# Kernel tuning notes

Measured on AMD Instinct MI355X. Metric: run time of the kernel, lower is better.

The kernel has to match this reference:

```python
import jax, jax.numpy as jnp
import numpy as np

N = 8192
D = 512


def setup_inputs() -> dict:
    key = jax.random.key(0)
    k1, k2, k3, k4 = jax.random.split(key, 4)
    U = jax.random.normal(k1, (N, D), dtype=jnp.float32)
    V = jax.random.normal(k2, (N, D), dtype=jnp.float32)
    M = jax.random.normal(k3, (N, N), dtype=jnp.float32)
    W = jax.random.uniform(k4, (N, N), dtype=jnp.float32)
    alpha = jnp.ones((1,), dtype=jnp.float32) * 0.1
    return {"U": U, "V": V, "M": M, "W": W, "alpha": alpha}


def reference(U, V, M, W, alpha):
    # Reconstruction term: sum((U V^T - M)^2)
    recon = U @ V.T                                  # (N, N) GEMM
    part1 = jnp.sum(jnp.square(recon - M))
    # Manifold term in closed form:
    # sum_{i,j} W[i,j] * ||U_i - V_j||^2
    #   = sum_i rowW_i ||U_i||^2 + sum_j colW_j ||V_j||^2 - 2 sum(W * U V^T)
    u_sq = jnp.sum(U * U, axis=1)                    # (N,)
    v_sq = jnp.sum(V * V, axis=1)                    # (N,)
    row_w = jnp.sum(W, axis=1)                       # (N,)
    col_w = jnp.sum(W, axis=0)                       # (N,)
    cross = jnp.sum(W * recon)
    part2 = alpha[0] * (jnp.dot(row_w, u_sq) + jnp.dot(col_w, v_sq) - 2.0 * cross)
    total = part1 + part2
    return total / (M.shape[0] * M.shape[1])
```

## Files before the change

### kernel.cpp

```cpp
#include <hip/hip_runtime.h>
#include <hip/hip_bf16.h>
#include <stdint.h>

#define N_DIM 8192
#define D_DIM 512
#define BM 128
#define BN 128
#define BK 64
#define RSTR 140

typedef __attribute__((ext_vector_type(8))) short bf16x8;
typedef __attribute__((ext_vector_type(4))) float f32x4;

__device__ __forceinline__ unsigned short f2bf(float f) {
    unsigned int x = __float_as_uint(f);
    x += 0x7fffu + ((x >> 16) & 1u);
    return (unsigned short)(x >> 16);
}
__device__ __forceinline__ float bf2f(unsigned short u) {
    return __uint_as_float(((unsigned int)u) << 16);
}

__global__ void __launch_bounds__(256) prep_kernel(
    const float* __restrict__ U, const float* __restrict__ V,
    unsigned short* __restrict__ Ub, unsigned short* __restrict__ Vb,
    float* __restrict__ usq, float* __restrict__ vsq)
{
    int row = blockIdx.x;
    const float* src;
    unsigned short* dst;
    float* sq;
    if (row < N_DIM) {
        src = U + (size_t)row * D_DIM;
        dst = Ub + (size_t)row * D_DIM;
        sq  = usq + row;
    } else {
        int r = row - N_DIM;
        src = V + (size_t)r * D_DIM;
        dst = Vb + (size_t)r * D_DIM;
        sq  = vsq + r;
    }
    int t = threadIdx.x;
    float2 v = *reinterpret_cast<const float2*>(src + 2 * t);
    float s = v.x * v.x + v.y * v.y;
    ushort2 b;
    b.x = f2bf(v.x);
    b.y = f2bf(v.y);
    *reinterpret_cast<ushort2*>(dst + 2 * t) = b;

    #pragma unroll
    for (int o = 32; o > 0; o >>= 1) s += __shfl_down(s, o, 64);
    __shared__ float red[4];
    if ((t & 63) == 0) red[t >> 6] = s;
    __syncthreads();
    if (t == 0) *sq = red[0] + red[1] + red[2] + red[3];
}

__global__ void __launch_bounds__(256, 2) fused_kernel(
    const unsigned short* __restrict__ Ub, const unsigned short* __restrict__ Vb,
    const float* __restrict__ Mg, const float* __restrict__ Wg,
    const float* __restrict__ usq, const float* __restrict__ vsq,
    double* __restrict__ acc)
{
    __shared__ alignas(16) char smem[BM * BK * 2 + BN * BK * 2];
    __shared__ alignas(16) unsigned short recs[BM * RSTR];
    __shared__ float red1[4], red2[4];
    char* As = smem;
    char* Bs = smem + BM * BK * 2;

    const int t    = threadIdx.x;
    const int lane = t & 63;
    const int wave = t >> 6;
    const int wm   = wave >> 1;
    const int wn   = wave & 1;

    const int bid    = blockIdx.x;
    const int tile_m = bid >> 6;
    const int tile_n = bid & 63;
    const int row0   = tile_m * BM;
    const int col0   = tile_n * BN;

    const f32x4 zero = {0.f, 0.f, 0.f, 0.f};
    f32x4 a[4][4];
    #pragma unroll
    for (int i = 0; i < 4; ++i)
        #pragma unroll
        for (int j = 0; j < 4; ++j) a[i][j] = zero;

    auto As3 = (__attribute__((address_space(3))) char*)As;
    auto Bs3 = (__attribute__((address_space(3))) char*)Bs;

    for (int kt = 0; kt < D_DIM / BK; ++kt) {
        const int k0 = kt * BK;
        #pragma unroll
        for (int c = 0; c < 4; ++c) {
            int s   = c * 256 + t;
            int row = s >> 3;
            int kg  = s & 7;
            int kgs = kg ^ (row & 7);
            __builtin_amdgcn_global_load_lds(
                (const __attribute__((address_space(1))) void*)(Ub + (size_t)(row0 + row) * D_DIM + k0 + kgs * 8),
                (__attribute__((address_space(3))) void*)(As3 + s * 16), 16, 0, 0);
            __builtin_amdgcn_global_load_lds(
                (const __attribute__((address_space(1))) void*)(Vb + (size_t)(col0 + row) * D_DIM + k0 + kgs * 8),
                (__attribute__((address_space(3))) void*)(Bs3 + s * 16), 16, 0, 0);
        }
        __syncthreads();

        #pragma unroll
        for (int kc = 0; kc < 2; ++kc) {
            bf16x8 af[4], bfr[4];
            const int kgw = kc * 4 + (lane >> 4);
            #pragma unroll
            for (int i = 0; i < 4; ++i) {
                int ra = wm * 64 + i * 16 + (lane & 15);
                af[i]  = *reinterpret_cast<const bf16x8*>(As + ra * (BK * 2) + ((kgw ^ (ra & 7)) * 16));
                int rb = wn * 64 + i * 16 + (lane & 15);
                bfr[i] = *reinterpret_cast<const bf16x8*>(Bs + rb * (BK * 2) + ((kgw ^ (rb & 7)) * 16));
            }
            #pragma unroll
            for (int i = 0; i < 4; ++i)
                #pragma unroll
                for (int j = 0; j < 4; ++j)
                    a[i][j] = __builtin_amdgcn_mfma_f32_16x16x32_bf16(af[i], bfr[j], a[i][j], 0, 0, 0);
        }
        __syncthreads();
    }

    const int rg = t >> 4;
    const int c8 = (t & 15) * 8;

    const f32x4 vs0 = *reinterpret_cast<const f32x4*>(vsq + col0 + c8);
    const f32x4 vs1 = *reinterpret_cast<const f32x4*>(vsq + col0 + c8 + 4);

    float s1 = 0.f, s2 = 0.f;

    f32x4 m0[3], m1[3], w0[3], w1[3];
    float us[3];

    auto issue = [&](int chunk, int slot) {
        int r = chunk * 16 + rg;
        const float* Mp = Mg + (size_t)(row0 + r) * N_DIM + col0 + c8;
        const float* Wp = Wg + (size_t)(row0 + r) * N_DIM + col0 + c8;
        m0[slot] = *reinterpret_cast<const f32x4*>(Mp);
        m1[slot] = *reinterpret_cast<const f32x4*>(Mp + 4);
        w0[slot] = *reinterpret_cast<const f32x4*>(Wp);
        w1[slot] = *reinterpret_cast<const f32x4*>(Wp + 4);
        us[slot] = usq[row0 + r];
    };

    issue(0, 0);
    issue(1, 1);
    issue(2, 2);

    #pragma unroll
    for (int i = 0; i < 4; ++i)
        #pragma unroll
        for (int j = 0; j < 4; ++j)
            #pragma unroll
            for (int q = 0; q < 4; ++q) {
                int r = wm * 64 + i * 16 + (lane >> 4) * 4 + q;
                int c = wn * 64 + j * 16 + (lane & 15);
                recs[r * RSTR + c] = f2bf(a[i][j][q]);
            }
    __syncthreads();

    #pragma unroll
    for (int chunk = 0; chunk < 8; ++chunk) {
        const int slot = chunk % 3;
        int r = chunk * 16 + rg;
        bf16x8 rb = *reinterpret_cast<const bf16x8*>(&recs[r * RSTR + c8]);
        f32x4 lm0 = m0[slot], lm1 = m1[slot], lw0 = w0[slot], lw1 = w1[slot];
        float lus = us[slot];
        if (chunk + 3 < 8) issue(chunk + 3, slot);
        #pragma unroll
        for (int c = 0; c < 4; ++c) {
            float rc = bf2f((unsigned short)rb[c]);
            float d  = rc - lm0[c];
            s1 = fmaf(d, d, s1);
            s2 = fmaf(lw0[c], lus + vs0[c] - 2.f * rc, s2);
        }
        #pragma unroll
        for (int c = 0; c < 4; ++c) {
            float rc = bf2f((unsigned short)rb[4 + c]);
            float d  = rc - lm1[c];
            s1 = fmaf(d, d, s1);
            s2 = fmaf(lw1[c], lus + vs1[c] - 2.f * rc, s2);
        }
    }

    #pragma unroll
    for (int o = 32; o > 0; o >>= 1) {
        s1 += __shfl_down(s1, o, 64);
        s2 += __shfl_down(s2, o, 64);
    }
    if (lane == 0) { red1[wave] = s1; red2[wave] = s2; }
    __syncthreads();
    if (t == 0) {
        double a1s = (double)red1[0] + red1[1] + red1[2] + red1[3];
        double a2s = (double)red2[0] + red2[1] + red2[2] + red2[3];
        atomicAdd(acc, a1s);
        atomicAdd(acc + 1, a2s);
    }
}

__global__ void finalize_kernel(const double* __restrict__ acc,
                                const float* __restrict__ alpha,
                                float* __restrict__ out)
{
    double tot = acc[0] + (double)alpha[0] * acc[1];
    out[0] = (float)(tot / ((double)N_DIM * (double)N_DIM));
}

extern "C" void kernel_launch(void* const* d_in, const int* in_sizes, int n_in,
                              void* d_out, int out_size, void* d_ws, size_t ws_size,
                              hipStream_t stream) {
    const float* U     = (const float*)d_in[0];
    const float* V     = (const float*)d_in[1];
    const float* Mg    = (const float*)d_in[2];
    const float* Wg    = (const float*)d_in[3];
    const float* alpha = (const float*)d_in[4];

    char* ws = (char*)d_ws;
    unsigned short* Ub = (unsigned short*)ws;
    unsigned short* Vb = (unsigned short*)(ws + 8u * 1024 * 1024);
    float* usq = (float*)(ws + 16u * 1024 * 1024);
    float* vsq = (float*)(ws + 16u * 1024 * 1024 + 32u * 1024);
    double* acc = (double*)(ws + 16u * 1024 * 1024 + 64u * 1024);

    hipMemsetAsync(acc, 0, 2 * sizeof(double), stream);
    prep_kernel<<<2 * N_DIM, 256, 0, stream>>>(U, V, Ub, Vb, usq, vsq);
    fused_kernel<<<(N_DIM / BM) * (N_DIM / BN), 256, 0, stream>>>(
        Ub, Vb, Mg, Wg, usq, vsq, acc);
    finalize_kernel<<<1, 1, 0, stream>>>(acc, alpha, (float*)d_out);
}
```

Baseline: 181.8 us.

## Reuse GEMM LDS for fp32 epilogue staging in two halves, raise occupancy

The separate bf16 staging buffer for the GEMM result is removed. The fp32 accumulators are now written into the existing A/B tile shared memory in two 64-row halves, using an XOR-swizzled layout, with barriers between the halves. This cuts LDS per block so launch bounds can ask for 3 blocks per CU. It also drops the bf16 rounding of the reconstruction in the epilogue. The M/W loads are reorganised into three 4-row register buffers so they overlap the dumps. The cost is higher register pressure from the 3-wave occupancy target, with a risk of spills.

```diff
diff --git a/kernel.cpp b/kernel.cpp
--- a/kernel.cpp
+++ b/kernel.cpp
@@ -7,7 +7,6 @@
 #define BM 128
 #define BN 128
 #define BK 64
-#define RSTR 140
 
 typedef __attribute__((ext_vector_type(8))) short bf16x8;
 typedef __attribute__((ext_vector_type(4))) float f32x4;
@@ -16,9 +15,6 @@
     unsigned int x = __float_as_uint(f);
     x += 0x7fffu + ((x >> 16) & 1u);
     return (unsigned short)(x >> 16);
-}
-__device__ __forceinline__ float bf2f(unsigned short u) {
-    return __uint_as_float(((unsigned int)u) << 16);
 }
 
 __global__ void __launch_bounds__(256) prep_kernel(
@@ -56,17 +52,17 @@
     if (t == 0) *sq = red[0] + red[1] + red[2] + red[3];
 }
 
-__global__ void __launch_bounds__(256, 2) fused_kernel(
+__global__ void __launch_bounds__(256, 3) fused_kernel(
     const unsigned short* __restrict__ Ub, const unsigned short* __restrict__ Vb,
     const float* __restrict__ Mg, const float* __restrict__ Wg,
     const float* __restrict__ usq, const float* __restrict__ vsq,
     double* __restrict__ acc)
 {
     __shared__ alignas(16) char smem[BM * BK * 2 + BN * BK * 2];
-    __shared__ alignas(16) unsigned short recs[BM * RSTR];
     __shared__ float red1[4], red2[4];
     char* As = smem;
     char* Bs = smem + BM * BK * 2;
+    float* recs = (float*)smem;
 
     const int t    = threadIdx.x;
     const int lane = t & 63;
@@ -127,67 +123,88 @@
         __syncthreads();
     }
 
-    const int rg = t >> 4;
-    const int c8 = (t & 15) * 8;
-
-    const f32x4 vs0 = *reinterpret_cast<const f32x4*>(vsq + col0 + c8);
-    const f32x4 vs1 = *reinterpret_cast<const f32x4*>(vsq + col0 + c8 + 4);
+    const int rloc = t >> 5;
+    const int cg   = t & 31;
+    const int c4   = cg * 4;
+    const f32x4 vs = *reinterpret_cast<const f32x4*>(vsq + col0 + c4);
 
     float s1 = 0.f, s2 = 0.f;
 
-    f32x4 m0[3], m1[3], w0[3], w1[3];
-    float us[3];
-
-    auto issue = [&](int chunk, int slot) {
-        int r = chunk * 16 + rg;
-        const float* Mp = Mg + (size_t)(row0 + r) * N_DIM + col0 + c8;
-        const float* Wp = Wg + (size_t)(row0 + r) * N_DIM + col0 + c8;
-        m0[slot] = *reinterpret_cast<const f32x4*>(Mp);
-        m1[slot] = *reinterpret_cast<const f32x4*>(Mp + 4);
-        w0[slot] = *reinterpret_cast<const f32x4*>(Wp);
-        w1[slot] = *reinterpret_cast<const f32x4*>(Wp + 4);
-        us[slot] = usq[row0 + r];
-    };
-
-    issue(0, 0);
-    issue(1, 1);
-    issue(2, 2);
-
-    #pragma unroll
-    for (int i = 0; i < 4; ++i)
-        #pragma unroll
-        for (int j = 0; j < 4; ++j)
-            #pragma unroll
-            for (int q = 0; q < 4; ++q) {
-                int r = wm * 64 + i * 16 + (lane >> 4) * 4 + q;
-                int c = wn * 64 + j * 16 + (lane & 15);
-                recs[r * RSTR + c] = f2bf(a[i][j][q]);
-            }
-    __syncthreads();
-
-    #pragma unroll
-    for (int chunk = 0; chunk < 8; ++chunk) {
-        const int slot = chunk % 3;
-        int r = chunk * 16 + rg;
-        bf16x8 rb = *reinterpret_cast<const bf16x8*>(&recs[r * RSTR + c8]);
-        f32x4 lm0 = m0[slot], lm1 = m1[slot], lw0 = w0[slot], lw1 = w1[slot];
-        float lus = us[slot];
-        if (chunk + 3 < 8) issue(chunk + 3, slot);
-        #pragma unroll
-        for (int c = 0; c < 4; ++c) {
-            float rc = bf2f((unsigned short)rb[c]);
-            float d  = rc - lm0[c];
-            s1 = fmaf(d, d, s1);
-            s2 = fmaf(lw0[c], lus + vs0[c] - 2.f * rc, s2);
-        }
-        #pragma unroll
-        for (int c = 0; c < 4; ++c) {
-            float rc = bf2f((unsigned short)rb[4 + c]);
-            float d  = rc - lm1[c];
-            s1 = fmaf(d, d, s1);
-            s2 = fmaf(lw1[c], lus + vs1[c] - 2.f * rc, s2);
-        }
-    }
+    f32x4 mA[4], wA[4]; float uA[4];
+    f32x4 mB[4], wB[4]; float uB[4];
+    f32x4 mC[4], wC[4]; float uC[4];
+
+    #define ISSUE(S, h, kk)                                                          \
+        do {                                                                         \
+            _Pragma("unroll")                                                        \
+            for (int b = 0; b < 4; ++b) {                                            \
+                int r    = rloc + ((kk) * 4 + b) * 8;                                \
+                int grow = row0 + (h) * 64 + r;                                      \
+                m##S[b] = *reinterpret_cast<const f32x4*>(Mg + (size_t)grow * N_DIM + col0 + c4); \
+                w##S[b] = *reinterpret_cast<const f32x4*>(Wg + (size_t)grow * N_DIM + col0 + c4); \
+                u##S[b] = usq[grow];                                                 \
+            }                                                                        \
+        } while (0)
+
+    #define CONSUME(S, kk)                                                           \
+        do {                                                                         \
+            _Pragma("unroll")                                                        \
+            for (int b = 0; b < 4; ++b) {                                            \
+                int r = rloc + ((kk) * 4 + b) * 8;                                   \
+                f32x4 rc = *reinterpret_cast<const f32x4*>(                          \
+                    &recs[r * 128 + ((cg ^ (r & 7)) << 2)]);                         \
+                _Pragma("unroll")                                                    \
+                for (int c = 0; c < 4; ++c) {                                        \
+                    float d = rc[c] - m##S[b][c];                                    \
+                    s1 = fmaf(d, d, s1);                                             \
+                    s2 = fmaf(w##S[b][c], u##S[b] + vs[c] - 2.f * rc[c], s2);        \
+                }                                                                    \
+            }                                                                        \
+        } while (0)
+
+    #define DUMP_HALF(h)                                                             \
+        do {                                                                         \
+            if (wm == (h)) {                                                         \
+                _Pragma("unroll")                                                    \
+                for (int i = 0; i < 4; ++i)                                          \
+                    _Pragma("unroll")                                                \
+                    for (int j = 0; j < 4; ++j)                                      \
+                        _Pragma("unroll")                                            \
+                        for (int q = 0; q < 4; ++q) {                                \
+                            int r = i * 16 + (lane >> 4) * 4 + q;                    \
+                            int c = wn * 64 + j * 16 + (lane & 15);                  \
+                            recs[r * 128 + ((((c >> 2) ^ (r & 7))) << 2) + (c & 3)]  \
+                                = a[i][j][q];                                        \
+                        }                                                            \
+            }                                                                        \
+        } while (0)
+
+    #define LGKM0_BAR() do { \
+        asm volatile("s_waitcnt lgkmcnt(0)" ::: "memory"); \
+        __builtin_amdgcn_s_barrier(); } while (0)
+
+    ISSUE(A, 0, 0);
+    ISSUE(B, 0, 1);
+    ISSUE(C, 1, 0);
+
+    DUMP_HALF(0);
+    LGKM0_BAR();
+
+    CONSUME(A, 0);
+    ISSUE(A, 1, 1);
+    CONSUME(B, 1);
+    LGKM0_BAR();
+
+    DUMP_HALF(1);
+    LGKM0_BAR();
+
+    CONSUME(C, 0);
+    CONSUME(A, 1);
+
+    #undef ISSUE
+    #undef CONSUME
+    #undef DUMP_HALF
+    #undef LGKM0_BAR
 
     #pragma unroll
     for (int o = 32; o > 0; o >>= 1) {
```

Result: slower. 292.9 us (+61.1%).
